# Kernel tuning notes

Hardware: AMD Instinct MI355X
Metric: run time of the kernel (lower is better)

Reference implementation:

```python
import jax, jax.numpy as jnp
import numpy as np

N_NODES = 50000
N_EDGES = 800000
IN_DIM = 128
HID = 32
HEADS = 4
OUT_DIM = 64
NEG_SLOPE = 0.2


def _glorot(key, shape):
    fan = shape[0] + shape[-1] if len(shape) > 1 else shape[-1]
    lim = jnp.sqrt(6.0 / fan)
    return jax.random.uniform(key, shape, jnp.float32, -lim, lim)


def setup_inputs() -> dict:
    key = jax.random.key(0)
    ks = jax.random.split(key, 10)
    x = jax.random.normal(ks[0], (N_NODES, IN_DIM), jnp.float32)
    edge_index = jax.random.randint(ks[1], (2, N_EDGES), 0, N_NODES, jnp.int32)
    # layer 1: in=IN_DIM, heads=HEADS, out=HID, concat
    W1 = _glorot(ks[2], (IN_DIM, HEADS * HID))
    a_src1 = _glorot(ks[3], (HEADS, HID))
    a_dst1 = _glorot(ks[4], (HEADS, HID))
    b1 = jnp.zeros((HEADS * HID,), jnp.float32)
    # layer 2: in=HEADS*HID, heads=1, out=OUT_DIM, mean
    W2 = _glorot(ks[5], (HEADS * HID, OUT_DIM))
    a_src2 = _glorot(ks[6], (1, OUT_DIM))
    a_dst2 = _glorot(ks[7], (1, OUT_DIM))
    b2 = jnp.zeros((OUT_DIM,), jnp.float32)
    return {"x": x, "edge_index": edge_index, "W1": W1, "a_src1": a_src1,
            "a_dst1": a_dst1, "b1": b1, "W2": W2, "a_src2": a_src2,
            "a_dst2": a_dst2, "b2": b2}


def gat_conv(x, src, dst, W, a_src, a_dst, bias, heads, out_ch, concat, num_nodes):
    # x: [N, in]; src/dst: [E] (self-loops already included)
    h = (x @ W).reshape(num_nodes, heads, out_ch)          # [N, H, F]
    alpha_s = jnp.einsum('nhf,hf->nh', h, a_src)           # [N, H]
    alpha_d = jnp.einsum('nhf,hf->nh', h, a_dst)
    e = alpha_s[src] + alpha_d[dst]                        # [E, H]
    e = jnp.where(e >= 0, e, NEG_SLOPE * e)                # leaky relu
    # segment softmax over destination neighborhoods
    e_max = jax.ops.segment_max(e, dst, num_segments=num_nodes)
    ex = jnp.exp(e - e_max[dst])
    denom = jax.ops.segment_sum(ex, dst, num_segments=num_nodes)
    alpha = ex / (denom[dst] + 1e-16)                      # [E, H]
    msg = h[src] * alpha[:, :, None]                       # [E, H, F]
    out = jax.ops.segment_sum(msg, dst, num_segments=num_nodes)  # [N, H, F]
    if concat:
        out = out.reshape(num_nodes, heads * out_ch)
    else:
        out = out.mean(axis=1)
    return out + bias


def reference(x, edge_index, W1, a_src1, a_dst1, b1, W2, a_src2, a_dst2, b2):
    n = x.shape[0]
    # PyG GATConv default add_self_loops=True
    loop = jnp.arange(n, dtype=edge_index.dtype)
    src = jnp.concatenate([edge_index[0], loop])
    dst = jnp.concatenate([edge_index[1], loop])
    h = gat_conv(x, src, dst, W1, a_src1, a_dst1, b1, HEADS, HID, True, n)
    h = jax.nn.relu(h)
    out = gat_conv(h, src, dst, W2, a_src2, a_dst2, b2, 1, OUT_DIM, False, n)
    return out
```

## Files before the change

kernel.cpp:

```cpp
#include <hip/hip_runtime.h>
#include <hip/hip_fp16.h>
#include <math.h>


#define NEG_SLOPE 0.2f
#define CAP 64
#define DEGS 32

typedef _Float16 f16x8 __attribute__((ext_vector_type(8)));
typedef float    f32x4 __attribute__((ext_vector_type(4)));

__device__ __forceinline__ float lrelu_exp(float e) {
    e = (e >= 0.f) ? e : NEG_SLOPE * e;
    return __expf(e);
}

__global__ __launch_bounds__(256) void prep_kernel(
    const float* __restrict__ W1, __half* __restrict__ w1t,
    int* __restrict__ deg, int degWords) {
    const int tid = blockIdx.x * 256 + threadIdx.x;
    if (tid < 16384) {
        const int k = tid >> 7, c = tid & 127;
        w1t[c * 128 + k] = __float2half(W1[k * 128 + c]);
    }
    const int idx = tid * 4;
    if (idx < degWords)
        *(int4*)&deg[idx] = (int4){0, 0, 0, 0};
}

__global__ __launch_bounds__(256, 4) void build_kernel(
    const float* __restrict__ x, const __half* __restrict__ w1t,
    const float* __restrict__ a_src1, const float* __restrict__ a_dst1,
    __half* __restrict__ h1h, float* __restrict__ as1, float* __restrict__ ad1,
    const int* __restrict__ src, const int* __restrict__ dst,
    int* __restrict__ deg, unsigned short* __restrict__ col,
    int N, int E, int Gs) {
    __shared__ __half hs[64 * 136];
    const int tid = threadIdx.x;

    if (blockIdx.x < Gs) {
        const int base = blockIdx.x * 1024 + tid * 4;
        int s[4], d[4];
        if (base + 4 <= E) {
            int4 a = *(const int4*)&src[base];
            int4 c = *(const int4*)&dst[base];
            s[0]=a.x; s[1]=a.y; s[2]=a.z; s[3]=a.w;
            d[0]=c.x; d[1]=c.y; d[2]=c.z; d[3]=c.w;
        } else {
#pragma unroll
            for (int u = 0; u < 4; ++u) {
                int i = base + u;
                if (i < E) { s[u] = src[i]; d[u] = dst[i]; }
                else       { s[u] = -1;     d[u] = -1; }
            }
        }
        int p[4];
#pragma unroll
        for (int u = 0; u < 4; ++u)
            if (d[u] >= 0) p[u] = atomicAdd(&deg[(size_t)d[u] * DEGS], 1);
#pragma unroll
        for (int u = 0; u < 4; ++u)
            if (d[u] >= 0 && p[u] < CAP)
                col[d[u] * CAP + p[u]] = (unsigned short)s[u];
        return;
    }

    const int w    = tid >> 6;
    const int lane = tid & 63;
    const int r16  = lane & 15;
    const int g4   = lane >> 4;
    const int nb   = (blockIdx.x - Gs) * 64;

    f16x8 bf[2][4];
#pragma unroll
    for (int ct = 0; ct < 2; ++ct) {
        const int c = w * 32 + ct * 16 + r16;
#pragma unroll
        for (int ks = 0; ks < 4; ++ks)
            bf[ct][ks] = *(const f16x8*)&w1t[c * 128 + ks * 32 + g4 * 8];
    }

    f32x4 acc[4][2];
#pragma unroll
    for (int rt = 0; rt < 4; ++rt)
#pragma unroll
        for (int ct = 0; ct < 2; ++ct)
            acc[rt][ct] = (f32x4){0.f, 0.f, 0.f, 0.f};

#pragma unroll
    for (int rt = 0; rt < 4; ++rt) {
        int gr = nb + rt * 16 + r16;
        if (gr >= N) gr = N - 1;
        const float* xp = x + (size_t)gr * 128 + g4 * 8;
        f16x8 af[4];
#pragma unroll
        for (int ks = 0; ks < 4; ++ks) {
            float4 u0 = *(const float4*)(xp + ks * 32);
            float4 u1 = *(const float4*)(xp + ks * 32 + 4);
            f16x8 a;
            a[0] = (_Float16)u0.x; a[1] = (_Float16)u0.y;
            a[2] = (_Float16)u0.z; a[3] = (_Float16)u0.w;
            a[4] = (_Float16)u1.x; a[5] = (_Float16)u1.y;
            a[6] = (_Float16)u1.z; a[7] = (_Float16)u1.w;
            af[ks] = a;
        }
#pragma unroll
        for (int ct = 0; ct < 2; ++ct)
#pragma unroll
            for (int ks = 0; ks < 4; ++ks)
                acc[rt][ct] = __builtin_amdgcn_mfma_f32_16x16x32_f16(
                    af[ks], bf[ct][ks], acc[rt][ct], 0, 0, 0);
    }

#pragma unroll
    for (int rt = 0; rt < 4; ++rt)
#pragma unroll
        for (int ct = 0; ct < 2; ++ct) {
            const int c = w * 32 + ct * 16 + r16;
#pragma unroll
            for (int i = 0; i < 4; ++i) {
                const int r = rt * 16 + g4 * 4 + i;
                hs[r * 136 + c] = __float2half(acc[rt][ct][i]);
            }
        }
    __syncthreads();

#pragma unroll
    for (int p = 0; p < 4; ++p) {
        const int idx = tid + p * 256;
        const int row = idx >> 4;
        const int c8  = (idx & 15) << 3;
        const int gn  = nb + row;
        if (gn < N)
            *(uint4*)&h1h[(size_t)gn * 128 + c8] =
                *(const uint4*)&hs[row * 136 + c8];
    }

    {
        const int row  = tid >> 2;
        const int head = tid & 3;
        const int gn   = nb + row;
        if (gn < N) {
            const __half* hp = &hs[row * 136 + head * 32];
            float s = 0.f, dv = 0.f;
#pragma unroll
            for (int f4 = 0; f4 < 8; ++f4) {
                float4 av = *(const float4*)&a_src1[head * 32 + f4 * 4];
                float4 bv = *(const float4*)&a_dst1[head * 32 + f4 * 4];
                float2 h01 = __half22float2(*(const __half2*)&hp[f4 * 4]);
                float2 h23 = __half22float2(*(const __half2*)&hp[f4 * 4 + 2]);
                s  += h01.x * av.x + h01.y * av.y + h23.x * av.z + h23.y * av.w;
                dv += h01.x * bv.x + h01.y * bv.y + h23.x * bv.z + h23.y * bv.w;
            }
            as1[(size_t)gn * 4 + head] = s;
            ad1[(size_t)gn * 4 + head] = dv;
        }
    }
}

__global__ __launch_bounds__(256) void agg1mm_kernel(
    const __half2* __restrict__ h1h2, const float* __restrict__ as1,
    const float* __restrict__ ad1, const float* __restrict__ b1,
    const float* __restrict__ W2, const float* __restrict__ a_src2,
    const float* __restrict__ a_dst2, const int* __restrict__ deg,
    const unsigned short* __restrict__ col,
    __half* __restrict__ h2h, float* __restrict__ as2, float* __restrict__ ad2,
    int N) {
    __shared__ float wls[4][4][68];
    __shared__ int   cls[4][64];
    __shared__ float hrs[4][128];
    __shared__ float part[16][64];
    const int tid = threadIdx.x;
    const int w = tid >> 6;
    const int lane = tid & 63;
    const int d = blockIdx.x * 4 + w;

    if (d < N) {
        const int hsel = lane >> 4;
        const float4 ad4 = *(const float4*)&ad1[4 * d];
        const float4 asd = *(const float4*)&as1[4 * d];
        const float adh = (hsel == 0) ? ad4.x : (hsel == 1) ? ad4.y
                        : (hsel == 2) ? ad4.z : ad4.w;
        const float ash = (hsel == 0) ? asd.x : (hsel == 1) ? asd.y
                        : (hsel == 2) ? asd.z : asd.w;
        const int dg = min(deg[(size_t)d * DEGS], CAP);
        const int dgp = (dg + 15) & ~15;
        const int beg = d * CAP;

        if (lane < dgp) {
            if (lane < dg) {
                int s = (int)col[beg + lane];
                cls[w][lane] = s;
                float4 a4 = *(const float4*)&as1[4 * s];
                wls[w][0][lane] = lrelu_exp(a4.x + ad4.x);
                wls[w][1][lane] = lrelu_exp(a4.y + ad4.y);
                wls[w][2][lane] = lrelu_exp(a4.z + ad4.z);
                wls[w][3][lane] = lrelu_exp(a4.w + ad4.w);
            } else {
                cls[w][lane] = 0;
                wls[w][0][lane] = 0.f;
                wls[w][1][lane] = 0.f;
                wls[w][2][lane] = 0.f;
                wls[w][3][lane] = 0.f;
            }
        }

        float wself = lrelu_exp(ash + adh);
        float2 vself = __half22float2(h1h2[((unsigned)d << 6) | (unsigned)lane]);
        float den = wself, accx = wself * vself.x, accy = wself * vself.y;

        for (int jj = 0; jj < dgp; jj += 16) {
            int4 c0 = *(const int4*)&cls[w][jj];
            int4 c1 = *(const int4*)&cls[w][jj + 4];
            int4 c2 = *(const int4*)&cls[w][jj + 8];
            int4 c3 = *(const int4*)&cls[w][jj + 12];
            int ss[16] = {c0.x, c0.y, c0.z, c0.w, c1.x, c1.y, c1.z, c1.w,
                          c2.x, c2.y, c2.z, c2.w, c3.x, c3.y, c3.z, c3.w};
            __half2 v[16];
#pragma unroll
            for (int u = 0; u < 16; ++u)
                v[u] = h1h2[(((unsigned)ss[u]) << 6) | (unsigned)lane];
            float4 w0 = *(const float4*)&wls[w][hsel][jj];
            float4 w1 = *(const float4*)&wls[w][hsel][jj + 4];
            float4 w2 = *(const float4*)&wls[w][hsel][jj + 8];
            float4 w3 = *(const float4*)&wls[w][hsel][jj + 12];
            float wt[16] = {w0.x, w0.y, w0.z, w0.w, w1.x, w1.y, w1.z, w1.w,
                            w2.x, w2.y, w2.z, w2.w, w3.x, w3.y, w3.z, w3.w};
#pragma unroll
            for (int u = 0; u < 16; ++u) {
                float2 vf = __half22float2(v[u]);
                den += wt[u];
                accx += wt[u] * vf.x;
                accy += wt[u] * vf.y;
            }
        }
        const float inv = 1.f / (den + 1e-16f);
        float2 bv = *(const float2*)&b1[lane * 2];
        float2 o;
        o.x = fmaxf(accx * inv + bv.x, 0.f);
        o.y = fmaxf(accy * inv + bv.y, 0.f);
        *(float2*)&hrs[w][lane * 2] = o;
    } else {
        hrs[w][lane * 2] = 0.f;
        hrs[w][lane * 2 + 1] = 0.f;
    }
    __syncthreads();

    float p0 = 0.f, p1 = 0.f, p2 = 0.f, p3 = 0.f;
#pragma unroll
    for (int kk = 0; kk < 32; kk += 4) {
        const int k = w * 32 + kk;
        float4 h0 = *(const float4*)&hrs[0][k];
        float4 h1 = *(const float4*)&hrs[1][k];
        float4 h2 = *(const float4*)&hrs[2][k];
        float4 h3 = *(const float4*)&hrs[3][k];
        float wv0 = W2[(k + 0) * 64 + lane];
        float wv1 = W2[(k + 1) * 64 + lane];
        float wv2 = W2[(k + 2) * 64 + lane];
        float wv3 = W2[(k + 3) * 64 + lane];
        p0 += h0.x * wv0 + h0.y * wv1 + h0.z * wv2 + h0.w * wv3;
        p1 += h1.x * wv0 + h1.y * wv1 + h1.z * wv2 + h1.w * wv3;
        p2 += h2.x * wv0 + h2.y * wv1 + h2.z * wv2 + h2.w * wv3;
        p3 += h3.x * wv0 + h3.y * wv1 + h3.z * wv2 + h3.w * wv3;
    }
    part[w * 4 + 0][lane] = p0;
    part[w * 4 + 1][lane] = p1;
    part[w * 4 + 2][lane] = p2;
    part[w * 4 + 3][lane] = p3;
    __syncthreads();

    if (d < N) {
        float h2f = part[0 * 4 + w][lane] + part[1 * 4 + w][lane] +
                    part[2 * 4 + w][lane] + part[3 * 4 + w][lane];
        h2h[((unsigned)d << 6) | (unsigned)lane] = __float2half(h2f);
        float s = h2f * a_src2[lane];
        float dv = h2f * a_dst2[lane];
        s += __shfl_down(s, 32); dv += __shfl_down(dv, 32);
        s += __shfl_down(s, 16); dv += __shfl_down(dv, 16);
        s += __shfl_down(s, 8);  dv += __shfl_down(dv, 8);
        s += __shfl_down(s, 4);  dv += __shfl_down(dv, 4);
        s += __shfl_down(s, 2);  dv += __shfl_down(dv, 2);
        s += __shfl_down(s, 1);  dv += __shfl_down(dv, 1);
        if (lane == 0) { as2[d] = s; ad2[d] = dv; }
    }
}

__global__ __launch_bounds__(256) void agg2_kernel(
    const __half* __restrict__ h2h, const float* __restrict__ as2,
    const float* __restrict__ ad2, const float* __restrict__ b2,
    const int* __restrict__ deg, const unsigned short* __restrict__ col,
    float* __restrict__ out, int N) {
    __shared__ int   cls[4][64];
    __shared__ float wl[4][64];
    const int lane = threadIdx.x & 63;
    const int w = threadIdx.x >> 6;
    const int d = blockIdx.x * 4 + w;
    if (d >= N) return;
    const int dg = min(deg[(size_t)d * DEGS], CAP);
    const int dgp = (dg + 15) & ~15;
    const int beg = d * CAP;
    const float adv = ad2[d];

    float wself = lrelu_exp(as2[d] + adv);
    float den = wself;
    float acc = wself * __half2float(h2h[((unsigned)d << 6) | (unsigned)lane]);

    if (lane < dgp) {
        if (lane < dg) {
            int s = (int)col[beg + lane];
            cls[w][lane] = s;
            wl[w][lane] = lrelu_exp(as2[s] + adv);
        } else {
            cls[w][lane] = 0;
            wl[w][lane] = 0.f;
        }
    }

    for (int jj = 0; jj < dgp; jj += 16) {
        int4 c0 = *(const int4*)&cls[w][jj];
        int4 c1 = *(const int4*)&cls[w][jj + 4];
        int4 c2 = *(const int4*)&cls[w][jj + 8];
        int4 c3 = *(const int4*)&cls[w][jj + 12];
        int ss[16] = {c0.x, c0.y, c0.z, c0.w, c1.x, c1.y, c1.z, c1.w,
                      c2.x, c2.y, c2.z, c2.w, c3.x, c3.y, c3.z, c3.w};
        __half v[16];
#pragma unroll
        for (int u = 0; u < 16; ++u)
            v[u] = h2h[(((unsigned)ss[u]) << 6) | (unsigned)lane];
        float4 w0 = *(const float4*)&wl[w][jj];
        float4 w1 = *(const float4*)&wl[w][jj + 4];
        float4 w2 = *(const float4*)&wl[w][jj + 8];
        float4 w3 = *(const float4*)&wl[w][jj + 12];
        float wt[16] = {w0.x, w0.y, w0.z, w0.w, w1.x, w1.y, w1.z, w1.w,
                        w2.x, w2.y, w2.z, w2.w, w3.x, w3.y, w3.z, w3.w};
#pragma unroll
        for (int u = 0; u < 16; ++u) {
            den += wt[u];
            acc += wt[u] * __half2float(v[u]);
        }
    }
    out[(size_t)d * 64 + lane] = acc / (den + 1e-16f) + b2[lane];
}

extern "C" void kernel_launch(void* const* d_in, const int* in_sizes, int n_in,
                              void* d_out, int out_size, void* d_ws, size_t ws_size,
                              hipStream_t stream) {
    const float* x      = (const float*)d_in[0];
    const int*   eidx   = (const int*)d_in[1];
    const float* W1     = (const float*)d_in[2];
    const float* a_src1 = (const float*)d_in[3];
    const float* a_dst1 = (const float*)d_in[4];
    const float* b1     = (const float*)d_in[5];
    const float* W2     = (const float*)d_in[6];
    const float* a_src2 = (const float*)d_in[7];
    const float* a_dst2 = (const float*)d_in[8];
    const float* b2     = (const float*)d_in[9];
    float* out = (float*)d_out;

    const int N = in_sizes[0] / 128;
    const int E = in_sizes[1] / 2;

    const int* src = eidx;
    const int* dst = eidx + E;

    float* ws_f = (float*)d_ws;
    float* as1 = ws_f;
    float* ad1 = as1 + (size_t)N * 4;
    float* as2 = ad1 + (size_t)N * 4;
    float* ad2 = as2 + (size_t)N;
    __half* h1h = (__half*)(ad2 + (size_t)N);
    __half* h2h = h1h + (size_t)N * 128;
    int* deg = (int*)(h2h + (size_t)N * 64);
    unsigned short* col = (unsigned short*)(deg + (size_t)N * DEGS);
    __half* w1t = (__half*)(col + (size_t)N * CAP);

    const int degWords = N * DEGS;
    const int Gp = (degWords / 4 + 255) / 256;
    const int Gs = (E + 1023) / 1024;
    const int Gg = (N + 63) / 64;

    prep_kernel<<<Gp, 256, 0, stream>>>(W1, w1t, deg, degWords);

    build_kernel<<<Gs + Gg, 256, 0, stream>>>(x, w1t, a_src1, a_dst1,
                                              h1h, as1, ad1,
                                              src, dst, deg, col, N, E, Gs);

    agg1mm_kernel<<<(N + 3) / 4, 256, 0, stream>>>(
        (const __half2*)h1h, as1, ad1, b1, W2, a_src2, a_dst2,
        deg, col, h2h, as2, ad2, N);

    agg2_kernel<<<(N + 3) / 4, 256, 0, stream>>>(h2h, as2, ad2, b2,
                                                 deg, col, out, N);
}
```

Measured before the change: 219.6 us.

## Split each wavefront into two half-waves gathering alternate neighbours with wider loads

Both aggregation kernels now split each 64-lane wavefront into two halves. Each half handles alternate neighbours, and each lane loads a wider vector per neighbour (8 or 4 bytes instead of 4 or 2). The two partial sums are combined with a cross-half shuffle, and padding drops from 16 to 8 neighbours. The aim is to halve the serial gather depth per node and raise bytes per load instruction, at the cost of an extra shuffle reduction and half the lanes sitting idle on the store. The edge-binning part of the build kernel also processes 8 edges per thread instead of 4, with half as many blocks.

```diff
diff --git a/kernel.cpp b/kernel.cpp
--- a/kernel.cpp
+++ b/kernel.cpp
@@ -39,27 +39,31 @@
     const int tid = threadIdx.x;
 
     if (blockIdx.x < Gs) {
-        const int base = blockIdx.x * 1024 + tid * 4;
-        int s[4], d[4];
-        if (base + 4 <= E) {
-            int4 a = *(const int4*)&src[base];
-            int4 c = *(const int4*)&dst[base];
-            s[0]=a.x; s[1]=a.y; s[2]=a.z; s[3]=a.w;
-            d[0]=c.x; d[1]=c.y; d[2]=c.z; d[3]=c.w;
+        const int base = blockIdx.x * 2048 + tid * 8;
+        int s[8], d[8];
+        if (base + 8 <= E) {
+            int4 a0 = *(const int4*)&src[base];
+            int4 a1 = *(const int4*)&src[base + 4];
+            int4 c0 = *(const int4*)&dst[base];
+            int4 c1 = *(const int4*)&dst[base + 4];
+            s[0]=a0.x; s[1]=a0.y; s[2]=a0.z; s[3]=a0.w;
+            s[4]=a1.x; s[5]=a1.y; s[6]=a1.z; s[7]=a1.w;
+            d[0]=c0.x; d[1]=c0.y; d[2]=c0.z; d[3]=c0.w;
+            d[4]=c1.x; d[5]=c1.y; d[6]=c1.z; d[7]=c1.w;
         } else {
 #pragma unroll
-            for (int u = 0; u < 4; ++u) {
+            for (int u = 0; u < 8; ++u) {
                 int i = base + u;
                 if (i < E) { s[u] = src[i]; d[u] = dst[i]; }
                 else       { s[u] = -1;     d[u] = -1; }
             }
         }
-        int p[4];
-#pragma unroll
-        for (int u = 0; u < 4; ++u)
+        int p[8];
+#pragma unroll
+        for (int u = 0; u < 8; ++u)
             if (d[u] >= 0) p[u] = atomicAdd(&deg[(size_t)d[u] * DEGS], 1);
 #pragma unroll
-        for (int u = 0; u < 4; ++u)
+        for (int u = 0; u < 8; ++u)
             if (d[u] >= 0 && p[u] < CAP)
                 col[d[u] * CAP + p[u]] = (unsigned short)s[u];
         return;
@@ -159,90 +163,95 @@
 }
 
 __global__ __launch_bounds__(256) void agg1mm_kernel(
-    const __half2* __restrict__ h1h2, const float* __restrict__ as1,
+    const __half* __restrict__ h1h, const float* __restrict__ as1,
     const float* __restrict__ ad1, const float* __restrict__ b1,
     const float* __restrict__ W2, const float* __restrict__ a_src2,
     const float* __restrict__ a_dst2, const int* __restrict__ deg,
     const unsigned short* __restrict__ col,
     __half* __restrict__ h2h, float* __restrict__ as2, float* __restrict__ ad2,
     int N) {
-    __shared__ float wls[4][4][68];
-    __shared__ int   cls[4][64];
+    __shared__ float wls[4][4][2][36];
+    __shared__ int   cls[4][2][32];
     __shared__ float hrs[4][128];
     __shared__ float part[16][64];
     const int tid = threadIdx.x;
     const int w = tid >> 6;
     const int lane = tid & 63;
+    const int q = lane & 31;
+    const int p = lane >> 5;
+    const int head = q >> 3;
     const int d = blockIdx.x * 4 + w;
 
     if (d < N) {
-        const int hsel = lane >> 4;
         const float4 ad4 = *(const float4*)&ad1[4 * d];
         const float4 asd = *(const float4*)&as1[4 * d];
-        const float adh = (hsel == 0) ? ad4.x : (hsel == 1) ? ad4.y
-                        : (hsel == 2) ? ad4.z : ad4.w;
-        const float ash = (hsel == 0) ? asd.x : (hsel == 1) ? asd.y
-                        : (hsel == 2) ? asd.z : asd.w;
+        const float adh = (head == 0) ? ad4.x : (head == 1) ? ad4.y
+                        : (head == 2) ? ad4.z : ad4.w;
+        const float ash = (head == 0) ? asd.x : (head == 1) ? asd.y
+                        : (head == 2) ? asd.z : asd.w;
         const int dg = min(deg[(size_t)d * DEGS], CAP);
-        const int dgp = (dg + 15) & ~15;
+        const int dgp = (dg + 7) & ~7;
         const int beg = d * CAP;
 
         if (lane < dgp) {
+            const int pp = lane & 1, hh = lane >> 1;
             if (lane < dg) {
                 int s = (int)col[beg + lane];
-                cls[w][lane] = s;
+                cls[w][pp][hh] = s;
                 float4 a4 = *(const float4*)&as1[4 * s];
-                wls[w][0][lane] = lrelu_exp(a4.x + ad4.x);
-                wls[w][1][lane] = lrelu_exp(a4.y + ad4.y);
-                wls[w][2][lane] = lrelu_exp(a4.z + ad4.z);
-                wls[w][3][lane] = lrelu_exp(a4.w + ad4.w);
+                wls[w][0][pp][hh] = lrelu_exp(a4.x + ad4.x);
+                wls[w][1][pp][hh] = lrelu_exp(a4.y + ad4.y);
+                wls[w][2][pp][hh] = lrelu_exp(a4.z + ad4.z);
+                wls[w][3][pp][hh] = lrelu_exp(a4.w + ad4.w);
             } else {
-                cls[w][lane] = 0;
-                wls[w][0][lane] = 0.f;
-                wls[w][1][lane] = 0.f;
-                wls[w][2][lane] = 0.f;
-                wls[w][3][lane] = 0.f;
+                cls[w][pp][hh] = 0;
+                wls[w][0][pp][hh] = 0.f;
+                wls[w][1][pp][hh] = 0.f;
+                wls[w][2][pp][hh] = 0.f;
+                wls[w][3][pp][hh] = 0.f;
             }
         }
 
-        float wself = lrelu_exp(ash + adh);
-        float2 vself = __half22float2(h1h2[((unsigned)d << 6) | (unsigned)lane]);
-        float den = wself, accx = wself * vself.x, accy = wself * vself.y;
-
-        for (int jj = 0; jj < dgp; jj += 16) {
-            int4 c0 = *(const int4*)&cls[w][jj];
-            int4 c1 = *(const int4*)&cls[w][jj + 4];
-            int4 c2 = *(const int4*)&cls[w][jj + 8];
-            int4 c3 = *(const int4*)&cls[w][jj + 12];
-            int ss[16] = {c0.x, c0.y, c0.z, c0.w, c1.x, c1.y, c1.z, c1.w,
-                          c2.x, c2.y, c2.z, c2.w, c3.x, c3.y, c3.z, c3.w};
-            __half2 v[16];
-#pragma unroll
-            for (int u = 0; u < 16; ++u)
-                v[u] = h1h2[(((unsigned)ss[u]) << 6) | (unsigned)lane];
-            float4 w0 = *(const float4*)&wls[w][hsel][jj];
-            float4 w1 = *(const float4*)&wls[w][hsel][jj + 4];
-            float4 w2 = *(const float4*)&wls[w][hsel][jj + 8];
-            float4 w3 = *(const float4*)&wls[w][hsel][jj + 12];
-            float wt[16] = {w0.x, w0.y, w0.z, w0.w, w1.x, w1.y, w1.z, w1.w,
-                            w2.x, w2.y, w2.z, w2.w, w3.x, w3.y, w3.z, w3.w};
-#pragma unroll
-            for (int u = 0; u < 16; ++u) {
-                float2 vf = __half22float2(v[u]);
-                den += wt[u];
-                accx += wt[u] * vf.x;
-                accy += wt[u] * vf.y;
+        float den = 0.f, a0 = 0.f, a1 = 0.f, a2 = 0.f, a3 = 0.f;
+        for (int jj = 0; jj < dgp; jj += 8) {
+            const int hb = jj >> 1;
+            int4 cs = *(const int4*)&cls[w][p][hb];
+            float4 wt = *(const float4*)&wls[w][head][p][hb];
+            int ss[4] = {cs.x, cs.y, cs.z, cs.w};
+            float wa[4] = {wt.x, wt.y, wt.z, wt.w};
+            uint2 v[4];
+#pragma unroll
+            for (int u = 0; u < 4; ++u)
+                v[u] = *(const uint2*)&h1h[((size_t)ss[u] << 7) + 4 * q];
+#pragma unroll
+            for (int u = 0; u < 4; ++u) {
+                float2 lo = __half22float2(*(const __half2*)&v[u].x);
+                float2 hi = __half22float2(*(const __half2*)&v[u].y);
+                den += wa[u];
+                a0 += wa[u] * lo.x; a1 += wa[u] * lo.y;
+                a2 += wa[u] * hi.x; a3 += wa[u] * hi.y;
             }
         }
+        den += __shfl_xor(den, 32);
+        a0 += __shfl_xor(a0, 32); a1 += __shfl_xor(a1, 32);
+        a2 += __shfl_xor(a2, 32); a3 += __shfl_xor(a3, 32);
+        const float wself = lrelu_exp(ash + adh);
+        uint2 sv = *(const uint2*)&h1h[((size_t)d << 7) + 4 * q];
+        float2 slo = __half22float2(*(const __half2*)&sv.x);
+        float2 shi = __half22float2(*(const __half2*)&sv.y);
+        den += wself;
+        a0 += wself * slo.x; a1 += wself * slo.y;
+        a2 += wself * shi.x; a3 += wself * shi.y;
         const float inv = 1.f / (den + 1e-16f);
-        float2 bv = *(const float2*)&b1[lane * 2];
-        float2 o;
-        o.x = fmaxf(accx * inv + bv.x, 0.f);
-        o.y = fmaxf(accy * inv + bv.y, 0.f);
-        *(float2*)&hrs[w][lane * 2] = o;
+        float4 bv = *(const float4*)&b1[4 * q];
+        float4 o;
+        o.x = fmaxf(a0 * inv + bv.x, 0.f);
+        o.y = fmaxf(a1 * inv + bv.y, 0.f);
+        o.z = fmaxf(a2 * inv + bv.z, 0.f);
+        o.w = fmaxf(a3 * inv + bv.w, 0.f);
+        if (p == 0) *(float4*)&hrs[w][4 * q] = o;
     } else {
-        hrs[w][lane * 2] = 0.f;
-        hrs[w][lane * 2 + 1] = 0.f;
+        if (p == 0) *(float4*)&hrs[w][4 * q] = (float4){0.f, 0.f, 0.f, 0.f};
     }
     __syncthreads();
 
@@ -290,56 +299,66 @@
     const float* __restrict__ ad2, const float* __restrict__ b2,
     const int* __restrict__ deg, const unsigned short* __restrict__ col,
     float* __restrict__ out, int N) {
-    __shared__ int   cls[4][64];
-    __shared__ float wl[4][64];
+    __shared__ int   cls[4][2][32];
+    __shared__ float wl[4][2][36];
     const int lane = threadIdx.x & 63;
     const int w = threadIdx.x >> 6;
+    const int q = lane & 31;
+    const int p = lane >> 5;
     const int d = blockIdx.x * 4 + w;
     if (d >= N) return;
     const int dg = min(deg[(size_t)d * DEGS], CAP);
-    const int dgp = (dg + 15) & ~15;
+    const int dgp = (dg + 7) & ~7;
     const int beg = d * CAP;
     const float adv = ad2[d];
 
-    float wself = lrelu_exp(as2[d] + adv);
-    float den = wself;
-    float acc = wself * __half2float(h2h[((unsigned)d << 6) | (unsigned)lane]);
-
     if (lane < dgp) {
+        const int pp = lane & 1, hh = lane >> 1;
         if (lane < dg) {
             int s = (int)col[beg + lane];
-            cls[w][lane] = s;
-            wl[w][lane] = lrelu_exp(as2[s] + adv);
+            cls[w][pp][hh] = s;
+            wl[w][pp][hh] = lrelu_exp(as2[s] + adv);
         } else {
-            cls[w][lane] = 0;
-            wl[w][lane] = 0.f;
-        }
-    }
-
-    for (int jj = 0; jj < dgp; jj += 16) {
-        int4 c0 = *(const int4*)&cls[w][jj];
-        int4 c1 = *(const int4*)&cls[w][jj + 4];
-        int4 c2 = *(const int4*)&cls[w][jj + 8];
-        int4 c3 = *(const int4*)&cls[w][jj + 12];
-        int ss[16] = {c0.x, c0.y, c0.z, c0.w, c1.x, c1.y, c1.z, c1.w,
-                      c2.x, c2.y, c2.z, c2.w, c3.x, c3.y, c3.z, c3.w};
-        __half v[16];
-#pragma unroll
-        for (int u = 0; u < 16; ++u)
-            v[u] = h2h[(((unsigned)ss[u]) << 6) | (unsigned)lane];
-        float4 w0 = *(const float4*)&wl[w][jj];
-        float4 w1 = *(const float4*)&wl[w][jj + 4];
-        float4 w2 = *(const float4*)&wl[w][jj + 8];
-        float4 w3 = *(const float4*)&wl[w][jj + 12];
-        float wt[16] = {w0.x, w0.y, w0.z, w0.w, w1.x, w1.y, w1.z, w1.w,
-                        w2.x, w2.y, w2.z, w2.w, w3.x, w3.y, w3.z, w3.w};
-#pragma unroll
-        for (int u = 0; u < 16; ++u) {
-            den += wt[u];
-            acc += wt[u] * __half2float(v[u]);
-        }
-    }
-    out[(size_t)d * 64 + lane] = acc / (den + 1e-16f) + b2[lane];
+            cls[w][pp][hh] = 0;
+            wl[w][pp][hh] = 0.f;
+        }
+    }
+
+    float den = 0.f, ax = 0.f, ay = 0.f;
+    for (int jj = 0; jj < dgp; jj += 8) {
+        const int hb = jj >> 1;
+        int4 cs = *(const int4*)&cls[w][p][hb];
+        float4 wt = *(const float4*)&wl[w][p][hb];
+        int ss[4] = {cs.x, cs.y, cs.z, cs.w};
+        float wa[4] = {wt.x, wt.y, wt.z, wt.w};
+        unsigned v[4];
+#pragma unroll
+        for (int u = 0; u < 4; ++u)
+            v[u] = *(const unsigned*)&h2h[((size_t)ss[u] << 6) + 2 * q];
+#pragma unroll
+        for (int u = 0; u < 4; ++u) {
+            float2 f = __half22float2(*(const __half2*)&v[u]);
+            den += wa[u];
+            ax += wa[u] * f.x;
+            ay += wa[u] * f.y;
+        }
+    }
+    den += __shfl_xor(den, 32);
+    ax += __shfl_xor(ax, 32);
+    ay += __shfl_xor(ay, 32);
+    const float wself = lrelu_exp(as2[d] + adv);
+    unsigned sv = *(const unsigned*)&h2h[((size_t)d << 6) + 2 * q];
+    float2 sf = __half22float2(*(const __half2*)&sv);
+    den += wself;
+    ax += wself * sf.x;
+    ay += wself * sf.y;
+    if (p == 0) {
+        const float inv = 1.f / (den + 1e-16f);
+        float2 o;
+        o.x = ax * inv + b2[2 * q];
+        o.y = ay * inv + b2[2 * q + 1];
+        *(float2*)&out[(size_t)d * 64 + 2 * q] = o;
+    }
 }
 
 extern "C" void kernel_launch(void* const* d_in, const int* in_sizes, int n_in,
@@ -376,7 +395,7 @@
 
     const int degWords = N * DEGS;
     const int Gp = (degWords / 4 + 255) / 256;
-    const int Gs = (E + 1023) / 1024;
+    const int Gs = (E + 2047) / 2048;
     const int Gg = (N + 63) / 64;
 
     prep_kernel<<<Gp, 256, 0, stream>>>(W1, w1t, deg, degWords);
@@ -386,7 +405,7 @@
                                               src, dst, deg, col, N, E, Gs);
 
     agg1mm_kernel<<<(N + 3) / 4, 256, 0, stream>>>(
-        (const __half2*)h1h, as1, ad1, b1, W2, a_src2, a_dst2,
+        h1h, as1, ad1, b1, W2, a_src2, a_dst2,
         deg, col, h2h, as2, ad2, N);
 
     agg2_kernel<<<(N + 3) / 4, 256, 0, stream>>>(h2h, as2, ad2, b2,
```

Result: no change. 218.5 us (-0.5%).
